# Kernel tuning notes

Measured on AMD Instinct MI355X. Metric: run time of the kernel, lower is better.

The kernel has to match this reference:

```python
import jax, jax.numpy as jnp
import numpy as np

N = 40000      # num nodes
M = 640000     # num edges (avg degree 16)
D = 128        # hidden_size / embed_dim
H = 8          # attn_num_heads
HD = D // H    # head_dim = 16
FF = 512       # tfmr_ff_sz
LN_EPS = 1e-5
SOFTMAX_EPS = 1e-16  # matches torch_geometric.utils.softmax


def setup_inputs() -> dict:
    key = jax.random.key(0)
    ks = jax.random.split(key, 8)
    s = 0.05
    return {
        "node_states": jax.random.normal(ks[0], (N, D), dtype=jnp.float32),
        "edges": jax.random.randint(ks[1], (2, M), 0, N, dtype=jnp.int64),
        # SelfAttentionMessageLayer params (F.linear convention: W is (out, in))
        "w_qkv": jax.random.normal(ks[2], (3 * D, D), dtype=jnp.float32) * s,
        "b_qkv": jnp.zeros((3 * D,), dtype=jnp.float32),
        "w_out": jax.random.normal(ks[3], (D, D), dtype=jnp.float32) * s,
        "b_out": jnp.zeros((D,), dtype=jnp.float32),
        # TransformerUpdateLayer params
        "w1": jax.random.normal(ks[4], (FF, D), dtype=jnp.float32) * s,
        "b1": jnp.zeros((FF,), dtype=jnp.float32),
        "w2": jax.random.normal(ks[5], (D, FF), dtype=jnp.float32) * s,
        "b2": jnp.zeros((D,), dtype=jnp.float32),
        "g1": jnp.ones((D,), dtype=jnp.float32),
        "beta1": jnp.zeros((D,), dtype=jnp.float32),
        "g2": jnp.ones((D,), dtype=jnp.float32),
        "beta2": jnp.zeros((D,), dtype=jnp.float32),
    }


def _layer_norm(x, g, b):
    mu = jnp.mean(x, axis=-1, keepdims=True)
    var = jnp.mean(jnp.square(x - mu), axis=-1, keepdims=True)
    return g * (x - mu) * jax.lax.rsqrt(var + LN_EPS) + b


def _sparse_self_attention(node_states, edges, w_qkv, b_qkv, w_out, b_out):
    num_nodes = node_states.shape[0]
    src, tgt = edges[0], edges[1]
    qkv = node_states @ w_qkv.T + b_qkv                      # (N, 3D)
    q, k, v = jnp.split(qkv, 3, axis=1)                      # each (N, D)
    q_e = q[tgt]                                             # (M, D) gather by target
    k_e = k[src]                                             # (M, D) gather by source
    v_e = v[src]                                             # (M, D)
    m = q_e.shape[0]
    # per-edge, per-head scaled dot-product scores
    scores = (q_e * k_e).reshape(m, H, HD).sum(-1) * (HD ** -0.5)   # (M, H)
    # scatter-softmax over edges sharing the same target node
    smax = jax.ops.segment_max(scores, tgt, num_segments=num_nodes)  # (N, H)
    smax = jnp.where(jnp.isfinite(smax), smax, 0.0)                  # empty segments
    ex = jnp.exp(scores - smax[tgt])                                 # (M, H)
    ssum = jax.ops.segment_sum(ex, tgt, num_segments=num_nodes)      # (N, H)
    attn_w = ex / (ssum[tgt] + SOFTMAX_EPS)                          # (M, H)
    # weighted scatter-add aggregation
    msg = (v_e.reshape(m, H, HD) * attn_w[:, :, None]).reshape(m, D)  # (M, D)
    agg = jax.ops.segment_sum(msg, tgt, num_segments=num_nodes)      # (N, D)
    return agg @ w_out.T + b_out


def _update(messages, node_states, w1, b1, w2, b2, g1, beta1, g2, beta2):
    x = _layer_norm(node_states + messages, g1, beta1)
    ff = jax.nn.relu(x @ w1.T + b1) @ w2.T + b2
    return _layer_norm(x + ff, g2, beta2)


def reference(node_states, edges, w_qkv, b_qkv, w_out, b_out,
              w1, b1, w2, b2, g1, beta1, g2, beta2):
    old_node_states = node_states
    # layer_timesteps = [1]: one message/update layer, one propagation step
    messages = _sparse_self_attention(node_states, edges, w_qkv, b_qkv, w_out, b_out)
    node_states = _update(messages, node_states, w1, b1, w2, b2, g1, beta1, g2, beta2)
    return (node_states, old_node_states)
```

## Files before the change

### kernel.cpp

```cpp
#include <hip/hip_runtime.h>
#include <hip/hip_bf16.h>
#include <math.h>

#define D_DIM 128
#define FF_DIM 512
#define BCAP 64

typedef __attribute__((ext_vector_type(8))) short bf16x8;
typedef __attribute__((ext_vector_type(4))) float f32x4;
typedef __attribute__((ext_vector_type(2))) float f32x2;
typedef __attribute__((ext_vector_type(4))) unsigned short u16x4;

__device__ __forceinline__ short f2bf(float f) {
    union { float f; unsigned u; } x; x.f = f;
    unsigned r = x.u + 0x7FFF + ((x.u >> 16) & 1);
    return (short)(r >> 16);
}
__device__ __forceinline__ float bf2f(short s) {
    union { unsigned u; float f; } x;
    x.u = ((unsigned)(unsigned short)s) << 16;
    return x.f;
}
__device__ __forceinline__ float lof(unsigned u) {
    union { unsigned u; float f; } x; x.u = u << 16; return x.f;
}
__device__ __forceinline__ float hif(unsigned u) {
    union { unsigned u; float f; } x; x.u = u & 0xFFFF0000u; return x.f;
}
__device__ __forceinline__ unsigned char f2fp8(float v) {
    return (unsigned char)(__builtin_amdgcn_cvt_pk_fp8_f32(v, v, 0, false) & 0xFF);
}

__device__ __forceinline__ void load_lds16(const short* g, short* l) {
    __builtin_amdgcn_global_load_lds(
        (const __attribute__((address_space(1))) unsigned int*)g,
        (__attribute__((address_space(3))) unsigned int*)l, 16, 0, 0);
}

template<int OUT_BF16, int RELU>
__global__ __launch_bounds__(256) void gemm_mfma(
    const short* __restrict__ A, const short* __restrict__ B,
    const float* __restrict__ bias, void* __restrict__ C,
    int Nc, int K)
{
    __shared__ short lA[2][128 * 32];
    __shared__ short lB[2][128 * 32];

    const int tid  = threadIdx.x;
    const int lane = tid & 63;
    const int wave = tid >> 6;
    const int wr = wave >> 1, wc = wave & 1;
    const int row0 = blockIdx.y * 128;
    const int col0 = blockIdx.x * 128;
    const int fr = lane & 15;
    const int fq = lane >> 4;
    const int sw = (fr >> 1) & 3;
    const int rdoff = (fq ^ sw) * 8;

    const int c0c = tid,        r0 = c0c >> 2, qg0 = (c0c & 3) ^ ((r0 >> 1) & 3);
    const int c1c = 256 + tid,  r1 = c1c >> 2, qg1 = (c1c & 3) ^ ((r1 >> 1) & 3);

#define STAGE_G(buf, kk) { \
    load_lds16(A + (size_t)(row0 + r0) * K + (kk) + qg0 * 8, &lA[buf][c0c * 8]); \
    load_lds16(B + (size_t)(col0 + r0) * K + (kk) + qg0 * 8, &lB[buf][c0c * 8]); \
    load_lds16(A + (size_t)(row0 + r1) * K + (kk) + qg1 * 8, &lA[buf][c1c * 8]); \
    load_lds16(B + (size_t)(col0 + r1) * K + (kk) + qg1 * 8, &lB[buf][c1c * 8]); }

    f32x4 acc[4][4] = {};
    const int nk = K >> 5;

    STAGE_G(0, 0)
    __syncthreads();
    int cur = 0;
    for (int t = 0; t < nk; ++t) {
        if (t + 1 < nk) STAGE_G(cur ^ 1, (t + 1) * 32)

        bf16x8 af[4], bfr[4];
#pragma unroll
        for (int m = 0; m < 4; ++m)
            af[m] = *(const bf16x8*)&lA[cur][(wr * 64 + m * 16 + fr) * 32 + rdoff];
#pragma unroll
        for (int n2 = 0; n2 < 4; ++n2)
            bfr[n2] = *(const bf16x8*)&lB[cur][(wc * 64 + n2 * 16 + fr) * 32 + rdoff];
#pragma unroll
        for (int m = 0; m < 4; ++m)
#pragma unroll
            for (int n2 = 0; n2 < 4; ++n2)
                acc[m][n2] = __builtin_amdgcn_mfma_f32_16x16x32_bf16(
                    af[m], bfr[n2], acc[m][n2], 0, 0, 0);
        __syncthreads();
        cur ^= 1;
    }
#undef STAGE_G

#pragma unroll
    for (int m = 0; m < 4; ++m) {
        int r = row0 + wr * 64 + m * 16 + fq * 4;
#pragma unroll
        for (int n2 = 0; n2 < 4; ++n2) {
            int c = col0 + wc * 64 + n2 * 16 + fr;
            float bb = bias[c];
#pragma unroll
            for (int j = 0; j < 4; ++j) {
                float v = acc[m][n2][j] + bb;
                if (RELU) v = fmaxf(v, 0.0f);
                if (OUT_BF16)
                    ((short*)C)[(size_t)(r + j) * Nc + c] = f2bf(v);
                else
                    ((float*)C)[(size_t)(r + j) * Nc + c] = v;
            }
        }
    }
}

__global__ __launch_bounds__(256) void qkv_gemm(
    const short* __restrict__ A, const short* __restrict__ B,
    const float* __restrict__ bias, void* __restrict__ C, int K)
{
    __shared__ short lA[2][128 * 32];
    __shared__ short lB[2][128 * 32];

    const int b = blockIdx.x;
    const int tid = threadIdx.x;
    const int lane = tid & 63;
    const int wave = tid >> 6;
    const int wr = wave >> 1, wc = wave & 1;
    const int row0 = (b / 3) * 128;
    const int col0 = (b % 3) * 128;
    const int fr = lane & 15;
    const int fq = lane >> 4;
    const int sw = (fr >> 1) & 3;
    const int rdoff = (fq ^ sw) * 8;

    const int c0c = tid,        r0 = c0c >> 2, qg0 = (c0c & 3) ^ ((r0 >> 1) & 3);
    const int c1c = 256 + tid,  r1 = c1c >> 2, qg1 = (c1c & 3) ^ ((r1 >> 1) & 3);

#define STAGE_G(buf, kk) { \
    load_lds16(A + (size_t)(row0 + r0) * K + (kk) + qg0 * 8, &lA[buf][c0c * 8]); \
    load_lds16(B + (size_t)(col0 + r0) * K + (kk) + qg0 * 8, &lB[buf][c0c * 8]); \
    load_lds16(A + (size_t)(row0 + r1) * K + (kk) + qg1 * 8, &lA[buf][c1c * 8]); \
    load_lds16(B + (size_t)(col0 + r1) * K + (kk) + qg1 * 8, &lB[buf][c1c * 8]); }

    f32x4 acc[4][4] = {};
    const int nk = K >> 5;

    STAGE_G(0, 0)
    __syncthreads();
    int cur = 0;
    for (int t = 0; t < nk; ++t) {
        if (t + 1 < nk) STAGE_G(cur ^ 1, (t + 1) * 32)

        bf16x8 af[4], bfr[4];
#pragma unroll
        for (int m = 0; m < 4; ++m)
            af[m] = *(const bf16x8*)&lA[cur][(wr * 64 + m * 16 + fr) * 32 + rdoff];
#pragma unroll
        for (int n2 = 0; n2 < 4; ++n2)
            bfr[n2] = *(const bf16x8*)&lB[cur][(wc * 64 + n2 * 16 + fr) * 32 + rdoff];
#pragma unroll
        for (int m = 0; m < 4; ++m)
#pragma unroll
            for (int n2 = 0; n2 < 4; ++n2)
                acc[m][n2] = __builtin_amdgcn_mfma_f32_16x16x32_bf16(
                    af[m], bfr[n2], acc[m][n2], 0, 0, 0);
        __syncthreads();
        cur ^= 1;
    }
#undef STAGE_G

#pragma unroll
    for (int m = 0; m < 4; ++m) {
        int r = row0 + wr * 64 + m * 16 + fq * 4;
#pragma unroll
        for (int n2 = 0; n2 < 4; ++n2) {
            int c = col0 + wc * 64 + n2 * 16 + fr;
            float bb = bias[c];
#pragma unroll
            for (int j = 0; j < 4; ++j) {
                float v = acc[m][n2][j] + bb;
                if (col0 == 0) {
                    ((short*)C)[(size_t)(r + j) * 256 + c] = f2bf(v);
                } else {
                    size_t byteoff = (size_t)(r + j) * 512 +
                        (col0 == 128 ? 256 + (c - 128) : 384 + (c - 256));
                    ((unsigned char*)C)[byteoff] = f2fp8(v);
                }
            }
        }
    }
}

template<int KD, int RES_BF, int OUT_BF>
__global__ __launch_bounds__(256) void gemm_ln(
    const short* __restrict__ A, const short* __restrict__ B,
    const float* __restrict__ bias, const void* __restrict__ res,
    const float* __restrict__ gamma, const float* __restrict__ beta,
    float* __restrict__ out32, short* __restrict__ outbf, int n)
{
    __shared__ short lA[2][64 * 32];
    __shared__ short lB[2][128 * 32];
    __shared__ float sums[64][2], sqs[64][2];
    __shared__ float muA[64], rsA[64];

    const int tid  = threadIdx.x;
    const int lane = tid & 63;
    const int wave = tid >> 6;
    const int wr = wave >> 1, wc = wave & 1;
    const int row0 = blockIdx.x * 64;
    const int fr = lane & 15;
    const int fq = lane >> 4;
    const int sw = (fr >> 1) & 3;
    const int rdoff = (fq ^ sw) * 8;

    const int ra = tid >> 2,        qa = (tid & 3) ^ ((ra >> 1) & 3);
    const int cb0 = tid,       rb0 = cb0 >> 2, qb0 = (cb0 & 3) ^ ((rb0 >> 1) & 3);
    const int cb1 = 256 + tid, rb1 = cb1 >> 2, qb1 = (cb1 & 3) ^ ((rb1 >> 1) & 3);

#define STAGE_L(buf, kk) { \
    load_lds16(A + (size_t)(row0 + ra) * KD + (kk) + qa * 8,  &lA[buf][tid * 8]); \
    load_lds16(B + (size_t)rb0 * KD + (kk) + qb0 * 8, &lB[buf][cb0 * 8]); \
    load_lds16(B + (size_t)rb1 * KD + (kk) + qb1 * 8, &lB[buf][cb1 * 8]); }

    f32x4 acc[2][4] = {};
    const int nk = KD >> 5;

    STAGE_L(0, 0)
    __syncthreads();
    int cur = 0;
    for (int t = 0; t < nk; ++t) {
        if (t + 1 < nk) STAGE_L(cur ^ 1, (t + 1) * 32)

        bf16x8 af[2], bfr[4];
#pragma unroll
        for (int m = 0; m < 2; ++m)
            af[m] = *(const bf16x8*)&lA[cur][(wr * 32 + m * 16 + fr) * 32 + rdoff];
#pragma unroll
        for (int n2 = 0; n2 < 4; ++n2)
            bfr[n2] = *(const bf16x8*)&lB[cur][(wc * 64 + n2 * 16 + fr) * 32 + rdoff];
#pragma unroll
        for (int m = 0; m < 2; ++m)
#pragma unroll
            for (int n2 = 0; n2 < 4; ++n2)
                acc[m][n2] = __builtin_amdgcn_mfma_f32_16x16x32_bf16(
                    af[m], bfr[n2], acc[m][n2], 0, 0, 0);
        __syncthreads();
        cur ^= 1;
    }
#undef STAGE_L

    float bicol[4], gcol[4], bcol[4];
#pragma unroll
    for (int n2 = 0; n2 < 4; ++n2) {
        int c = wc * 64 + n2 * 16 + fr;
        bicol[n2] = bias[c]; gcol[n2] = gamma[c]; bcol[n2] = beta[c];
    }

#pragma unroll
    for (int m = 0; m < 2; ++m) {
#pragma unroll
        for (int j = 0; j < 4; ++j) {
            int rl = wr * 32 + m * 16 + fq * 4 + j;
            int rg = row0 + rl;
            float ps = 0.0f, pq = 0.0f;
#pragma unroll
            for (int n2 = 0; n2 < 4; ++n2) {
                float v = acc[m][n2][j] + bicol[n2];
                if (rg < n) {
                    size_t ri = (size_t)rg * 128 + wc * 64 + n2 * 16 + fr;
                    v += RES_BF ? bf2f(((const short*)res)[ri])
                                : ((const float*)res)[ri];
                }
                acc[m][n2][j] = v;
                ps += v; pq += v * v;
            }
            ps += __shfl_xor(ps, 1); ps += __shfl_xor(ps, 2);
            ps += __shfl_xor(ps, 4); ps += __shfl_xor(ps, 8);
            pq += __shfl_xor(pq, 1); pq += __shfl_xor(pq, 2);
            pq += __shfl_xor(pq, 4); pq += __shfl_xor(pq, 8);
            if (fr == 0) { sums[rl][wc] = ps; sqs[rl][wc] = pq; }
        }
    }
    __syncthreads();
    if (tid < 64) {
        float s = sums[tid][0] + sums[tid][1];
        float q = sqs[tid][0] + sqs[tid][1];
        float mu = s * (1.0f / 128.0f);
        float var = q * (1.0f / 128.0f) - mu * mu;
        muA[tid] = mu;
        rsA[tid] = rsqrtf(var + 1e-5f);
    }
    __syncthreads();

#pragma unroll
    for (int m = 0; m < 2; ++m) {
#pragma unroll
        for (int j = 0; j < 4; ++j) {
            int rl = wr * 32 + m * 16 + fq * 4 + j;
            int rg = row0 + rl;
            float mu = muA[rl], rs = rsA[rl];
#pragma unroll
            for (int n2 = 0; n2 < 4; ++n2) {
                int c = wc * 64 + n2 * 16 + fr;
                float o = gcol[n2] * (acc[m][n2][j] - mu) * rs + bcol[n2];
                if (OUT_BF) {
                    outbf[(size_t)rg * 128 + c] = (rg < n) ? f2bf(o) : (short)0;
                } else {
                    if (rg < n) out32[(size_t)rg * 128 + c] = o;
                }
            }
        }
    }
}

__global__ __launch_bounds__(256) void prep_kernel(
    const float* __restrict__ ns, short* __restrict__ nsbf,
    float* __restrict__ out_old, int n_elems, int mp_elems,
    const float* w0, const float* w1, const float* w2, const float* w3,
    short* o0, short* o1, short* o2, short* o3,
    int c0, int c1, int c2, int c3,
    const int* __restrict__ e_src, const int* __restrict__ e_tgt,
    int* __restrict__ counts, int* __restrict__ csr_src, int m_edges)
{
    int i = blockIdx.x * 256 + threadIdx.x;
    int i4 = i * 4;
    if (i4 < mp_elems) {
        if (i4 < n_elems) {
            float4 v = *(const float4*)(ns + i4);
            *(float4*)(out_old + i4) = v;
            u16x4 b;
            b.x = (unsigned short)f2bf(v.x); b.y = (unsigned short)f2bf(v.y);
            b.z = (unsigned short)f2bf(v.z); b.w = (unsigned short)f2bf(v.w);
            *(u16x4*)(nsbf + i4) = b;
        } else {
            u16x4 z = {0, 0, 0, 0};
            *(u16x4*)(nsbf + i4) = z;
        }
    }
    if (i < c0) o0[i] = f2bf(w0[i]);
    if (i < c1) o1[i] = f2bf(w1[i]);
    if (i < c2) o2[i] = f2bf(w2[i]);
    if (i < c3) o3[i] = f2bf(w3[i]);
    if (i < m_edges) {
        int t = e_tgt[i];
        int s = e_src[i];
        int pos = atomicAdd(&counts[t], 1);
        if (pos < BCAP) csr_src[(size_t)t * BCAP + pos] = s;
    }
}

template<int NG>
__device__ __forceinline__ void attn_fast(
    int cnt, int e, int mysrc,
    const unsigned char* kb, const unsigned char* vb,
    f32x2 q01, f32x2 q23, f32x2 q45, f32x2 q67,
    float& l, f32x2& A01, f32x2& A23, f32x2& A45, f32x2& A67)
{
    uint2 kr[NG]; float sc[NG]; int si[NG];
#pragma unroll
    for (int G = 0; G < NG; ++G) {
        if (4 * G < cnt) {
            int idx = 4 * G + e; if (idx >= cnt) idx = cnt - 1;
            si[G] = __shfl(mysrc, idx);
            kr[G] = *(const uint2*)(kb + (size_t)si[G] * 512);
        }
    }
    float mloc = -INFINITY;
#pragma unroll
    for (int G = 0; G < NG; ++G) {
        if (4 * G < cnt) {
            f32x2 s2 = q01 * __builtin_amdgcn_cvt_pk_f32_fp8(kr[G].x, 0);
            s2 += q23 * __builtin_amdgcn_cvt_pk_f32_fp8(kr[G].x, 1);
            s2 += q45 * __builtin_amdgcn_cvt_pk_f32_fp8(kr[G].y, 0);
            s2 += q67 * __builtin_amdgcn_cvt_pk_f32_fp8(kr[G].y, 1);
            float s = s2.x + s2.y;
            s += __shfl_xor(s, 4);
            sc[G] = (4 * G + e < cnt) ? s : -INFINITY;
            mloc = fmaxf(mloc, sc[G]);
        }
    }
    mloc = fmaxf(mloc, __shfl_xor(mloc, 1));
    mloc = fmaxf(mloc, __shfl_xor(mloc, 2));
#pragma unroll
    for (int G = 0; G < NG; ++G) {
        if (4 * G < cnt) {
            float p = exp2f(sc[G] - mloc);
            sc[G] = p;
            l += p;
        }
    }
    uint2 vr[NG];
#pragma unroll
    for (int G = 0; G < NG; ++G) {
        if (4 * G < cnt)
            vr[G] = *(const uint2*)(vb + (size_t)si[G] * 512);
    }
#pragma unroll
    for (int G = 0; G < NG; ++G) {
        if (4 * G < cnt) {
            f32x2 pv = {sc[G], sc[G]};
            A01 += pv * __builtin_amdgcn_cvt_pk_f32_fp8(vr[G].x, 0);
            A23 += pv * __builtin_amdgcn_cvt_pk_f32_fp8(vr[G].x, 1);
            A45 += pv * __builtin_amdgcn_cvt_pk_f32_fp8(vr[G].y, 0);
            A67 += pv * __builtin_amdgcn_cvt_pk_f32_fp8(vr[G].y, 1);
        }
    }
}

__global__ __launch_bounds__(256) void attn_kernel(
    const short* __restrict__ qkv, const int* __restrict__ counts,
    const int* __restrict__ csr_src, short* __restrict__ agg, int n, int mp)
{
    int node = blockIdx.x * 4 + (threadIdx.x >> 6);
    int lane = threadIdx.x & 63;
    if (node >= mp) return;
    const int hh = lane >> 2;
    const int e  = lane & 3;
    unsigned* outp = (unsigned*)(agg + (size_t)node * 128 + hh * 8 + e * 2);

    int cnt = 0;
    if (node < n) {
        cnt = counts[node];
        if (cnt > BCAP) cnt = BCAP;
    }
    if (cnt == 0) { *outp = 0u; return; }
    const int beg = node * BCAP;

    const float SC = 0.25f * 1.44269504088896340736f;
    const uint4 qd = *(const uint4*)(qkv + (size_t)node * 256 + hh * 8);
    f32x2 q01 = {lof(qd.x) * SC, hif(qd.x) * SC};
    f32x2 q23 = {lof(qd.y) * SC, hif(qd.y) * SC};
    f32x2 q45 = {lof(qd.z) * SC, hif(qd.z) * SC};
    f32x2 q67 = {lof(qd.w) * SC, hif(qd.w) * SC};

    const unsigned char* kb = (const unsigned char*)qkv + 256 + hh * 8;
    const unsigned char* vb = (const unsigned char*)qkv + 384 + hh * 8;

    float l = 0.0f;
    f32x2 A01 = {0, 0}, A23 = {0, 0}, A45 = {0, 0}, A67 = {0, 0};

    int mysrc = csr_src[beg + ((lane < cnt) ? lane : (cnt - 1))];

    if (cnt <= 16) {
        attn_fast<4>(cnt, e, mysrc, kb, vb, q01, q23, q45, q67,
                     l, A01, A23, A45, A67);
    } else if (cnt <= 32) {
        attn_fast<8>(cnt, e, mysrc, kb, vb, q01, q23, q45, q67,
                     l, A01, A23, A45, A67);
    } else {
        float m = -INFINITY;
        uint2 kA, vA;
        {
            int sA = csr_src[beg + ((e < cnt) ? e : 0)];
            kA = *(const uint2*)(kb + (size_t)sA * 512);
            vA = *(const uint2*)(vb + (size_t)sA * 512);
        }
        for (int g = 0; g < cnt; g += 4) {
            uint2 kB = kA, vB = vA;
            if (g + 4 < cnt) {
                int t = g + 4 + e;
                int sB = csr_src[beg + ((t < cnt) ? t : 0)];
                kB = *(const uint2*)(kb + (size_t)sB * 512);
                vB = *(const uint2*)(vb + (size_t)sB * 512);
            }
            f32x2 s2 = q01 * __builtin_amdgcn_cvt_pk_f32_fp8(kA.x, 0);
            s2 += q23 * __builtin_amdgcn_cvt_pk_f32_fp8(kA.x, 1);
            s2 += q45 * __builtin_amdgcn_cvt_pk_f32_fp8(kA.y, 0);
            s2 += q67 * __builtin_amdgcn_cvt_pk_f32_fp8(kA.y, 1);
            float s = s2.x + s2.y;
            s += __shfl_xor(s, 4);
            float scv = (g + e < cnt) ? s : -INFINITY;
            float gm = fmaxf(scv, __shfl_xor(scv, 1));
            gm = fmaxf(gm, __shfl_xor(gm, 2));
            float mnew = fmaxf(m, gm);
            float corr = exp2f(m - mnew);
            float p = exp2f(scv - mnew);
            l = fmaf(l, corr, p);
            f32x2 cv = {corr, corr}, pv = {p, p};
            A01 = A01 * cv + pv * __builtin_amdgcn_cvt_pk_f32_fp8(vA.x, 0);
            A23 = A23 * cv + pv * __builtin_amdgcn_cvt_pk_f32_fp8(vA.x, 1);
            A45 = A45 * cv + pv * __builtin_amdgcn_cvt_pk_f32_fp8(vA.y, 0);
            A67 = A67 * cv + pv * __builtin_amdgcn_cvt_pk_f32_fp8(vA.y, 1);
            m = mnew;
            kA = kB; vA = vB;
        }
    }

    float a0 = A01.x, a1 = A01.y, a2 = A23.x, a3 = A23.y;
    float a4 = A45.x, a5 = A45.y, a6 = A67.x, a7 = A67.y;

    l  += __shfl_xor(l, 1);
    a0 += __shfl_xor(a0, 1); a1 += __shfl_xor(a1, 1);
    a2 += __shfl_xor(a2, 1); a3 += __shfl_xor(a3, 1);
    a4 += __shfl_xor(a4, 1); a5 += __shfl_xor(a5, 1);
    a6 += __shfl_xor(a6, 1); a7 += __shfl_xor(a7, 1);
    l  += __shfl_xor(l, 2);
    a0 += __shfl_xor(a0, 2); a1 += __shfl_xor(a1, 2);
    a2 += __shfl_xor(a2, 2); a3 += __shfl_xor(a3, 2);
    a4 += __shfl_xor(a4, 2); a5 += __shfl_xor(a5, 2);
    a6 += __shfl_xor(a6, 2); a7 += __shfl_xor(a7, 2);

    float inv = 1.0f / l;
    float o0, o1;
    if (e == 0)      { o0 = a0; o1 = a1; }
    else if (e == 1) { o0 = a2; o1 = a3; }
    else if (e == 2) { o0 = a4; o1 = a5; }
    else             { o0 = a6; o1 = a7; }
    *outp = ((unsigned)(unsigned short)f2bf(o1 * inv) << 16) |
            (unsigned)(unsigned short)f2bf(o0 * inv);
}

extern "C" void kernel_launch(void* const* d_in, const int* in_sizes, int n_in,
                              void* d_out, int out_size, void* d_ws, size_t ws_size,
                              hipStream_t stream)
{
    const float* node_states = (const float*)d_in[0];
    const int*   edges       = (const int*)d_in[1];
    const float* w_qkv = (const float*)d_in[2];
    const float* b_qkv = (const float*)d_in[3];
    const float* w_out = (const float*)d_in[4];
    const float* b_out = (const float*)d_in[5];
    const float* w1    = (const float*)d_in[6];
    const float* b1    = (const float*)d_in[7];
    const float* w2    = (const float*)d_in[8];
    const float* b2    = (const float*)d_in[9];
    const float* g1    = (const float*)d_in[10];
    const float* beta1 = (const float*)d_in[11];
    const float* g2    = (const float*)d_in[12];
    const float* beta2 = (const float*)d_in[13];

    const int N  = in_sizes[0] / D_DIM;
    const int M  = in_sizes[1] / 2;
    const int MP = ((N + 127) / 128) * 128;
    const int* e_src = edges;
    const int* e_tgt = edges + M;

    float* out_new = (float*)d_out;
    float* out_old = (float*)d_out + (size_t)N * D_DIM;

    size_t off = 0;
    auto alloc = [&](size_t bytes) -> void* {
        void* p = (char*)d_ws + off;
        off += (bytes + 255) & ~(size_t)255;
        return p;
    };
    short* ns_bf   = (short*)alloc((size_t)MP * D_DIM * 2);
    char*  region  = (char*)alloc((size_t)MP * 512);
    short* qkv_pk  = (short*)region;
    short* xbuf_bf = (short*)region;
    short* agg_bf  = (short*)alloc((size_t)MP * D_DIM * 2);
    short* ff1_bf  = (short*)alloc((size_t)MP * FF_DIM * 2);
    short* wqkv_bf = (short*)alloc((size_t)384 * 128 * 2);
    short* wout_bf = (short*)alloc((size_t)128 * 128 * 2);
    short* w1_bf   = (short*)alloc((size_t)512 * 128 * 2);
    short* w2_bf   = (short*)alloc((size_t)128 * 512 * 2);
    int* counts    = (int*)alloc((size_t)N * 4);
    int* csr_src   = (int*)alloc((size_t)N * BCAP * 4);
    (void)ws_size;

    hipMemsetAsync(counts, 0, (size_t)N * 4, stream);

    prep_kernel<<<(MP * D_DIM / 4 + 255) / 256, 256, 0, stream>>>(
        node_states, ns_bf, out_old, N * D_DIM, MP * D_DIM,
        w_qkv, w_out, w1, w2, wqkv_bf, wout_bf, w1_bf, w2_bf,
        384 * 128, 128 * 128, 512 * 128, 128 * 512,
        e_src, e_tgt, counts, csr_src, M);

    qkv_gemm<<<3 * (MP / 128), 256, 0, stream>>>(ns_bf, wqkv_bf, b_qkv,
                                                 qkv_pk, 128);
    attn_kernel<<<MP / 4, 256, 0, stream>>>(qkv_pk, counts, csr_src,
                                            agg_bf, N, MP);
    gemm_ln<128, 1, 1><<<MP / 64, 256, 0, stream>>>(
        agg_bf, wout_bf, b_out, ns_bf, g1, beta1,
        (float*)nullptr, xbuf_bf, N);
    {
        dim3 grid(FF_DIM / 128, MP / 128);
        gemm_mfma<1, 1><<<grid, 256, 0, stream>>>(xbuf_bf, w1_bf, b1,
                                                  ff1_bf, FF_DIM, 128);
    }
    gemm_ln<512, 1, 0><<<MP / 64, 256, 0, stream>>>(
        ff1_bf, w2_bf, b2, xbuf_bf, g2, beta2, out_new, (short*)nullptr, N);
}
```

Measured before the change: 173.0 us.

## Fuse edge bucketing into QKV GEMM launch and inline counts into buckets

Removes the separate memset of the count array. The prep kernel now zeroes one count slot per node inside the bucket array, with the count stored at index 0 of each 64-int bucket and capacity reduced to 63. The edge scatter moves out of the prep kernel into extra blocks of the QKV GEMM launch, so the atomic scatter runs alongside the GEMM tiles. In the attention kernel the count and the source indices now sit in the same cache line. The trade-offs are that degrees above 63 are truncated instead of above 64, and that the atomics and the GEMM now compete for resources in the same launch.

```diff
diff --git a/kernel.cpp b/kernel.cpp
--- a/kernel.cpp
+++ b/kernel.cpp
@@ -4,7 +4,8 @@
 
 #define D_DIM 128
 #define FF_DIM 512
-#define BCAP 64
+#define BSTRIDE 64
+#define BCAP 63
 
 typedef __attribute__((ext_vector_type(8))) short bf16x8;
 typedef __attribute__((ext_vector_type(4))) float f32x4;
@@ -113,15 +114,30 @@
     }
 }
 
-__global__ __launch_bounds__(256) void qkv_gemm(
+__global__ __launch_bounds__(256) void qkv_scatter(
     const short* __restrict__ A, const short* __restrict__ B,
-    const float* __restrict__ bias, void* __restrict__ C, int K)
+    const float* __restrict__ bias, void* __restrict__ C, int K,
+    const int* __restrict__ e_src, const int* __restrict__ e_tgt,
+    int* __restrict__ csr, int m_edges, int ngemm)
 {
     __shared__ short lA[2][128 * 32];
     __shared__ short lB[2][128 * 32];
 
     const int b = blockIdx.x;
     const int tid = threadIdx.x;
+
+    if (b >= ngemm) {
+        int i = (b - ngemm) * 256 + tid;
+        if (i < m_edges) {
+            int t = e_tgt[i];
+            int s = e_src[i];
+            int* bkt = csr + (size_t)t * BSTRIDE;
+            int pos = atomicAdd(bkt, 1);
+            if (pos < BCAP) bkt[1 + pos] = s;
+        }
+        return;
+    }
+
     const int lane = tid & 63;
     const int wave = tid >> 6;
     const int wr = wave >> 1, wc = wave & 1;
@@ -135,7 +151,7 @@
     const int c0c = tid,        r0 = c0c >> 2, qg0 = (c0c & 3) ^ ((r0 >> 1) & 3);
     const int c1c = 256 + tid,  r1 = c1c >> 2, qg1 = (c1c & 3) ^ ((r1 >> 1) & 3);
 
-#define STAGE_G(buf, kk) { \
+#define STAGE_Q(buf, kk) { \
     load_lds16(A + (size_t)(row0 + r0) * K + (kk) + qg0 * 8, &lA[buf][c0c * 8]); \
     load_lds16(B + (size_t)(col0 + r0) * K + (kk) + qg0 * 8, &lB[buf][c0c * 8]); \
     load_lds16(A + (size_t)(row0 + r1) * K + (kk) + qg1 * 8, &lA[buf][c1c * 8]); \
@@ -144,11 +160,11 @@
     f32x4 acc[4][4] = {};
     const int nk = K >> 5;
 
-    STAGE_G(0, 0)
+    STAGE_Q(0, 0)
     __syncthreads();
     int cur = 0;
     for (int t = 0; t < nk; ++t) {
-        if (t + 1 < nk) STAGE_G(cur ^ 1, (t + 1) * 32)
+        if (t + 1 < nk) STAGE_Q(cur ^ 1, (t + 1) * 32)
 
         bf16x8 af[4], bfr[4];
 #pragma unroll
@@ -166,7 +182,7 @@
         __syncthreads();
         cur ^= 1;
     }
-#undef STAGE_G
+#undef STAGE_Q
 
 #pragma unroll
     for (int m = 0; m < 4; ++m) {
@@ -318,8 +334,7 @@
     const float* w0, const float* w1, const float* w2, const float* w3,
     short* o0, short* o1, short* o2, short* o3,
     int c0, int c1, int c2, int c3,
-    const int* __restrict__ e_src, const int* __restrict__ e_tgt,
-    int* __restrict__ counts, int* __restrict__ csr_src, int m_edges)
+    int* __restrict__ csr, int n_nodes)
 {
     int i = blockIdx.x * 256 + threadIdx.x;
     int i4 = i * 4;
@@ -340,12 +355,7 @@
     if (i < c1) o1[i] = f2bf(w1[i]);
     if (i < c2) o2[i] = f2bf(w2[i]);
     if (i < c3) o3[i] = f2bf(w3[i]);
-    if (i < m_edges) {
-        int t = e_tgt[i];
-        int s = e_src[i];
-        int pos = atomicAdd(&counts[t], 1);
-        if (pos < BCAP) csr_src[(size_t)t * BCAP + pos] = s;
-    }
+    if (i < n_nodes) csr[(size_t)i * BSTRIDE] = 0;
 }
 
 template<int NG>
@@ -407,8 +417,8 @@
 }
 
 __global__ __launch_bounds__(256) void attn_kernel(
-    const short* __restrict__ qkv, const int* __restrict__ counts,
-    const int* __restrict__ csr_src, short* __restrict__ agg, int n, int mp)
+    const short* __restrict__ qkv, const int* __restrict__ csr,
+    short* __restrict__ agg, int n, int mp)
 {
     int node = blockIdx.x * 4 + (threadIdx.x >> 6);
     int lane = threadIdx.x & 63;
@@ -417,13 +427,13 @@
     const int e  = lane & 3;
     unsigned* outp = (unsigned*)(agg + (size_t)node * 128 + hh * 8 + e * 2);
 
+    const int* bkt = csr + (size_t)node * BSTRIDE;
     int cnt = 0;
     if (node < n) {
-        cnt = counts[node];
+        cnt = bkt[0];
         if (cnt > BCAP) cnt = BCAP;
     }
     if (cnt == 0) { *outp = 0u; return; }
-    const int beg = node * BCAP;
 
     const float SC = 0.25f * 1.44269504088896340736f;
     const uint4 qd = *(const uint4*)(qkv + (size_t)node * 256 + hh * 8);
@@ -438,7 +448,7 @@
     float l = 0.0f;
     f32x2 A01 = {0, 0}, A23 = {0, 0}, A45 = {0, 0}, A67 = {0, 0};
 
-    int mysrc = csr_src[beg + ((lane < cnt) ? lane : (cnt - 1))];
+    int mysrc = bkt[1 + ((lane < cnt) ? lane : (cnt - 1))];
 
     if (cnt <= 16) {
         attn_fast<4>(cnt, e, mysrc, kb, vb, q01, q23, q45, q67,
@@ -450,7 +460,7 @@
         float m = -INFINITY;
         uint2 kA, vA;
         {
-            int sA = csr_src[beg + ((e < cnt) ? e : 0)];
+            int sA = bkt[1 + ((e < cnt) ? e : 0)];
             kA = *(const uint2*)(kb + (size_t)sA * 512);
             vA = *(const uint2*)(vb + (size_t)sA * 512);
         }
@@ -458,7 +468,7 @@
             uint2 kB = kA, vB = vA;
             if (g + 4 < cnt) {
                 int t = g + 4 + e;
-                int sB = csr_src[beg + ((t < cnt) ? t : 0)];
+                int sB = bkt[1 + ((t < cnt) ? t : 0)];
                 kB = *(const uint2*)(kb + (size_t)sB * 512);
                 vB = *(const uint2*)(vb + (size_t)sB * 512);
             }
@@ -553,22 +563,23 @@
     short* wout_bf = (short*)alloc((size_t)128 * 128 * 2);
     short* w1_bf   = (short*)alloc((size_t)512 * 128 * 2);
     short* w2_bf   = (short*)alloc((size_t)128 * 512 * 2);
-    int* counts    = (int*)alloc((size_t)N * 4);
-    int* csr_src   = (int*)alloc((size_t)N * BCAP * 4);
+    int* csr       = (int*)alloc((size_t)N * BSTRIDE * 4);
     (void)ws_size;
-
-    hipMemsetAsync(counts, 0, (size_t)N * 4, stream);
 
     prep_kernel<<<(MP * D_DIM / 4 + 255) / 256, 256, 0, stream>>>(
         node_states, ns_bf, out_old, N * D_DIM, MP * D_DIM,
         w_qkv, w_out, w1, w2, wqkv_bf, wout_bf, w1_bf, w2_bf,
         384 * 128, 128 * 128, 512 * 128, 128 * 512,
-        e_src, e_tgt, counts, csr_src, M);
-
-    qkv_gemm<<<3 * (MP / 128), 256, 0, stream>>>(ns_bf, wqkv_bf, b_qkv,
-                                                 qkv_pk, 128);
-    attn_kernel<<<MP / 4, 256, 0, stream>>>(qkv_pk, counts, csr_src,
-                                            agg_bf, N, MP);
+        csr, N);
+
+    {
+        const int ngemm = 3 * (MP / 128);
+        const int nscat = (M + 255) / 256;
+        qkv_scatter<<<ngemm + nscat, 256, 0, stream>>>(
+            ns_bf, wqkv_bf, b_qkv, qkv_pk, 128,
+            e_src, e_tgt, csr, M, ngemm);
+    }
+    attn_kernel<<<MP / 4, 256, 0, stream>>>(qkv_pk, csr, agg_bf, N, MP);
     gemm_ln<128, 1, 1><<<MP / 64, 256, 0, stream>>>(
         agg_bf, wout_bf, b_out, ns_bf, g1, beta1,
         (float*)nullptr, xbuf_bf, N);
```

New measurement: 157.5 us. 8.9% less time.
